# Optimization experiments

Hardware: AMD Instinct MI355X
Metric: run time of the kernel (lower is better)

Reference implementation:

```python
import jax, jax.numpy as jnp
import numpy as np

OUTPUT_SIZES = [1, 3, 6, 8]  # SPP pyramid -> total KV length 110

def _bounds(n, out):
    # PyTorch AdaptiveMaxPool2d bin boundaries
    return [((i * n) // out, -((-(i + 1) * n) // out)) for i in range(out)]

def adaptive_max_pool2d(x, out):
    # x: [B, C, H, W] -> [B, C, out, out]
    B, C, H, W = x.shape
    rows = jnp.stack([x[:, :, s:e, :].max(axis=2) for s, e in _bounds(H, out)], axis=2)
    return jnp.stack([rows[:, :, :, s:e].max(axis=3) for s, e in _bounds(W, out)], axis=3)

def spp(x):
    # [B, C, H, W] -> [B, C, S] with S = sum(o*o) = 110
    B, C = x.shape[:2]
    return jnp.concatenate(
        [adaptive_max_pool2d(x, o).reshape(B, C, o * o) for o in OUTPUT_SIZES], axis=2)

def conv1x1(x, w):
    # 1x1 conv, no bias: w [O, C], x [B, C, H, W]
    return jnp.einsum('oc,bchw->bohw', w, x)

def setup_inputs() -> dict:
    key = jax.random.key(0)
    ks = jax.random.split(key, 6)
    B, C, H, W = 16, 512, 64, 64
    IC = C // 2
    x = jax.random.normal(ks[0], (B, C, H, W), jnp.float32)
    y = jax.random.normal(ks[1], (B, C, H, W), jnp.float32)
    sc = 1.0 / np.sqrt(C)
    w_phi = jax.random.normal(ks[2], (IC, C), jnp.float32) * sc
    w_theta = jax.random.normal(ks[3], (IC, C), jnp.float32) * sc
    w_g = jax.random.normal(ks[4], (IC, C), jnp.float32) * sc
    w_mask = jax.random.normal(ks[5], (C, IC), jnp.float32) * (1.0 / np.sqrt(IC))
    return {"x": x, "y": y, "w_phi": w_phi, "w_theta": w_theta,
            "w_g": w_g, "w_mask": w_mask}

def reference(x, y, w_phi, w_theta, w_g, w_mask):
    B, C, H, W = x.shape
    IC = w_phi.shape[0]
    N = H * W
    # Query: [B, N, IC]
    x_phi = conv1x1(x, w_phi).reshape(B, IC, N).transpose(0, 2, 1)
    # Keys/values from SPP-pooled y: [B, IC, S] / [B, S, IC]
    y_theta = spp(conv1x1(y, w_theta))
    y_g = spp(conv1x1(y, w_g)).transpose(0, 2, 1)
    # Attention with softmax over the QUERY axis (dim=1), as in the source
    attn = jax.nn.softmax(jnp.einsum('bnc,bcs->bns', x_phi, y_theta), axis=1)
    agg = jnp.einsum('bns,bsc->bnc', attn, y_g)          # [B, N, IC]
    agg = agg.transpose(0, 2, 1).reshape(B, IC, H, W)     # [B, IC, H, W]
    mask = conv1x1(agg, w_mask)                           # [B, C, H, W]
    return mask + x
```

## Files before the change

### kernel.cpp

```cpp
#include <hip/hip_runtime.h>

#define DI __device__ __forceinline__

typedef __attribute__((ext_vector_type(8))) __bf16 bf16x8;
typedef __attribute__((ext_vector_type(4))) float f32x4;

DI unsigned short f2bf(float x) {
  union { float f; unsigned u; } v; v.f = x;
  unsigned r = v.u + 0x7fffu + ((v.u >> 16) & 1u);
  return (unsigned short)(r >> 16);
}
DI float bf2f(unsigned short h) {
  union { unsigned u; float f; } v; v.u = ((unsigned)h) << 16;
  return v.f;
}
DI unsigned pack2(float a, float b) {
  return (unsigned)f2bf(a) | (((unsigned)f2bf(b)) << 16);
}

DI void gl_lds16(const void* g, void* l) {
  __builtin_amdgcn_global_load_lds(
      (const __attribute__((address_space(1))) void*)g,
      (__attribute__((address_space(3))) void*)l, 16, 0, 0);
}

__global__ __launch_bounds__(256) void p0w_transpose(
    const float* __restrict__ src, unsigned short* __restrict__ dst,
    const float* __restrict__ w_theta, const float* __restrict__ w_g,
    unsigned short* __restrict__ wTG)
{
  if (blockIdx.z == 16) {
    if (blockIdx.y < 2) {
      int e = ((blockIdx.y * 64 + blockIdx.x) * 256 + threadIdx.x) * 8;
      const float* s = (e < 131072) ? (w_theta + e) : (w_g + (e - 131072));
      float4 a = *(const float4*)s;
      float4 c = *(const float4*)(s + 4);
      uint4 u;
      u.x = pack2(a.x, a.y); u.y = pack2(a.z, a.w);
      u.z = pack2(c.x, c.y); u.w = pack2(c.z, c.w);
      *(uint4*)(wTG + e) = u;
    }
    return;
  }
  const int n0 = blockIdx.x * 64, c0 = blockIdx.y * 64, b = blockIdx.z;
  const int tid = threadIdx.x;
  __shared__ float T[64 * 65];
  #pragma unroll
  for (int p = 0; p < 4; ++p) {
    int r = p * 16 + (tid >> 4);
    int n4 = (tid & 15) << 2;
    *(float4*)&T[r * 65 + n4] =
        *(const float4*)(src + ((size_t)(b * 512 + c0 + r)) * 4096 + n0 + n4);
  }
  __syncthreads();
  int n = tid >> 2, cc = (tid & 3) * 16;
  unsigned u[8];
  #pragma unroll
  for (int j = 0; j < 16; j += 2)
    u[j >> 1] = pack2(T[(cc + j) * 65 + n], T[(cc + j + 1) * 65 + n]);
  unsigned short* d = dst + ((size_t)(b * 4096 + n0 + n)) * 512 + c0 + cc;
  *(uint4*)(d) = make_uint4(u[0], u[1], u[2], u[3]);
  *(uint4*)(d + 8) = make_uint4(u[4], u[5], u[6], u[7]);
}

__constant__ int c_RS[18] = {0, 0,21,42, 0,10,21,32,42,53, 0,8,16,24,32,40,48,56};
__constant__ int c_RE[18] = {64, 22,43,64, 11,22,32,43,54,64, 8,16,24,32,40,48,56,64};

__global__ __launch_bounds__(256) void k1f_conv_pool(
    const unsigned short* __restrict__ yT, const unsigned short* __restrict__ wTG,
    unsigned short* __restrict__ Rbuf)
{
  const int tid = threadIdx.x;
  const int id = blockIdx.x;
  const int tile = (id & 7) * 16 + (id >> 3);
  const int mb = (tile & 3) * 128;
  const int nbt = tile >> 2;
  const int nb = nbt * 128;
  const int b  = blockIdx.y;
  const int lane = tid & 63, wv = tid >> 6;
  const int wm = (wv & 1) * 64, wn = (wv >> 1) * 64;
  const int l15 = lane & 15, l4 = lane >> 4;

  __shared__ __align__(16) char smem[33280];
  float* P = (float*)smem;

  f32x4 acc[4][4];
  #pragma unroll
  for (int i = 0; i < 4; ++i)
    #pragma unroll
    for (int j = 0; j < 4; ++j) acc[i][j] = f32x4{0.f, 0.f, 0.f, 0.f};

  auto stage = [&](int buf, int kb) {
    unsigned short* As = (unsigned short*)(smem + buf * 16384);
    unsigned short* Bs = As + 4096;
    #pragma unroll
    for (int p = 0; p < 2; ++p) {
      int chunk = (wv * 2 + p) * 64 + lane;
      int row = chunk >> 2, c16 = chunk & 3;
      gl_lds16(wTG + ((size_t)(mb + row)) * 512 + kb + c16 * 8,
               As + (wv * 2 + p) * 512);
      gl_lds16(yT + ((size_t)(b * 4096 + nb + row)) * 512 + kb + c16 * 8,
               Bs + (wv * 2 + p) * 512);
    }
  };

  stage(0, 0);
  __syncthreads();
  int cur = 0;
  for (int t = 0; t < 16; ++t) {
    if (t < 15) stage(cur ^ 1, (t + 1) * 32);
    const unsigned short* As = (const unsigned short*)(smem + cur * 16384);
    const unsigned short* Bs = As + 4096;
    bf16x8 af[4], bfr[4];
    #pragma unroll
    for (int i = 0; i < 4; ++i)
      af[i] = *(const bf16x8*)&As[(wm + i * 16 + l15) * 32 + l4 * 8];
    #pragma unroll
    for (int j = 0; j < 4; ++j)
      bfr[j] = *(const bf16x8*)&Bs[(wn + j * 16 + l15) * 32 + l4 * 8];
    #pragma unroll
    for (int i = 0; i < 4; ++i)
      #pragma unroll
      for (int j = 0; j < 4; ++j)
        acc[i][j] = __builtin_amdgcn_mfma_f32_16x16x32_bf16(af[i], bfr[j], acc[i][j], 0, 0, 0);
    __syncthreads();
    cur ^= 1;
  }

  const int hloc = wv >> 1;
  #pragma unroll
  for (int pass = 0; pass < 2; ++pass) {
    __syncthreads();
    if (hloc == pass) {
      #pragma unroll
      for (int i = 0; i < 4; ++i)
        #pragma unroll
        for (int j = 0; j < 4; ++j)
          #pragma unroll
          for (int r = 0; r < 4; ++r)
            P[(wm + i * 16 + l4 * 4 + r) * 65 + j * 16 + l15] = acc[i][j][r];
    }
    __syncthreads();
    const int o = tid & 127;
    size_t rbase = (((size_t)(b * 64 + nbt * 2 + pass)) * 18) * 512 + mb + o;
    if (tid < 128) {
      float b0 = -3.4e38f, b1 = b0, b2 = b0, b3 = b0;
      #pragma unroll
      for (int w = 0; w < 64; ++w) {
        float v = P[o * 65 + w];
        b0 = fmaxf(b0, v);
        if (w < 22) b1 = fmaxf(b1, v);
        if (w >= 21 && w < 43) b2 = fmaxf(b2, v);
        if (w >= 42) b3 = fmaxf(b3, v);
      }
      Rbuf[rbase]           = f2bf(b0);
      Rbuf[rbase + 512]     = f2bf(b1);
      Rbuf[rbase + 2 * 512] = f2bf(b2);
      Rbuf[rbase + 3 * 512] = f2bf(b3);
    } else {
      float s6[6], s8[8];
      #pragma unroll
      for (int i = 0; i < 6; ++i) s6[i] = -3.4e38f;
      #pragma unroll
      for (int i = 0; i < 8; ++i) s8[i] = -3.4e38f;
      constexpr int R6S[6] = {0, 10, 21, 32, 42, 53};
      constexpr int R6E[6] = {11, 22, 32, 43, 54, 64};
      #pragma unroll
      for (int w = 0; w < 64; ++w) {
        float v = P[o * 65 + w];
        #pragma unroll
        for (int i = 0; i < 6; ++i)
          if (w >= R6S[i] && w < R6E[i]) s6[i] = fmaxf(s6[i], v);
        s8[w >> 3] = fmaxf(s8[w >> 3], v);
      }
      #pragma unroll
      for (int i = 0; i < 6; ++i) Rbuf[rbase + (size_t)(4 + i) * 512] = f2bf(s6[i]);
      #pragma unroll
      for (int i = 0; i < 8; ++i) Rbuf[rbase + (size_t)(10 + i) * 512] = f2bf(s8[i]);
    }
  }
}

__global__ __launch_bounds__(256) void k2_pool_final(
    const unsigned short* __restrict__ Rbuf, float* __restrict__ Pt,
    float* __restrict__ Pg)
{
  const int s = blockIdx.x, b = blockIdx.y, tid = threadIdx.x;
  size_t obase = ((size_t)(b * 128) + s) * 256 + tid;
  if (s >= 110) { Pt[obase] = 0.f; Pg[obase] = 0.f; return; }
  int he, wb;
  if (s == 0)      { he = 0; wb = 0; }
  else if (s < 10) { int i = s - 1;  he = 1 + i / 3;  wb = 1 + i % 3; }
  else if (s < 46) { int i = s - 10; he = 4 + i / 6;  wb = 4 + i % 6; }
  else             { int i = s - 46; he = 10 + i / 8; wb = 10 + i % 8; }
  float m0 = -3.4e38f, m1 = -3.4e38f;
  int e = c_RE[he];
  for (int h = c_RS[he]; h < e; ++h) {
    const unsigned short* r = Rbuf + (((size_t)(b * 64 + h)) * 18 + wb) * 512;
    m0 = fmaxf(m0, bf2f(r[tid]));
    m1 = fmaxf(m1, bf2f(r[tid + 256]));
  }
  Pt[obase] = m0;
  Pg[obase] = m1;
}

__global__ __launch_bounds__(256) void k3_fused(
    const float* __restrict__ Pt, const float* __restrict__ Pg,
    const float* __restrict__ w_phi, const float* __restrict__ w_mask,
    unsigned short* __restrict__ Kth, unsigned short* __restrict__ Ktl,
    unsigned short* __restrict__ Vb)
{
  __shared__ __align__(16) char sm3[51200];
  const int tid = threadIdx.x;
  const int tx = tid & 15, ty = tid >> 4;
  const int b = blockIdx.y;
  if (blockIdx.z == 0) {
    const int ct = blockIdx.x;
    const int c0 = tx * 4, s0 = ty * 8;
    float* Ls = (float*)sm3;
    float* Ws = Ls + 128 * 64;
    float acc[8][4] = {};
    for (int kc = 0; kc < 256; kc += 64) {
      #pragma unroll
      for (int j = 0; j < 8; ++j) {
        int flat = tid + 256 * j;
        int row = flat >> 4, k4 = (flat & 15) << 2;
        *(float4*)&Ls[row * 64 + k4] =
            *(const float4*)(Pt + ((size_t)(b * 128) + row) * 256 + kc + k4);
      }
      #pragma unroll
      for (int j = 0; j < 4; ++j) {
        int flat = tid + 256 * j;
        int row = flat >> 4, c4 = (flat & 15) << 2;
        *(float4*)&Ws[row * 68 + c4] =
            *(const float4*)(w_phi + (size_t)(kc + row) * 512 + ct * 64 + c4);
      }
      __syncthreads();
      for (int k = 0; k < 64; k += 4) {
        float4 wv[4];
        #pragma unroll
        for (int kk = 0; kk < 4; ++kk) wv[kk] = *(const float4*)&Ws[(k + kk) * 68 + c0];
        #pragma unroll
        for (int i = 0; i < 8; ++i) {
          float4 a = *(const float4*)&Ls[(s0 + i) * 64 + k];
          const float* ap = (const float*)&a;
          #pragma unroll
          for (int kk = 0; kk < 4; ++kk) {
            const float* wp = (const float*)&wv[kk];
            acc[i][0] += ap[kk] * wp[0];
            acc[i][1] += ap[kk] * wp[1];
            acc[i][2] += ap[kk] * wp[2];
            acc[i][3] += ap[kk] * wp[3];
          }
        }
      }
      __syncthreads();
    }
    #pragma unroll
    for (int i = 0; i < 8; ++i) {
      unsigned short hi[4]; float lo[4];
      #pragma unroll
      for (int j = 0; j < 4; ++j) { hi[j] = f2bf(acc[i][j]); lo[j] = acc[i][j] - bf2f(hi[j]); }
      size_t base = ((size_t)(b * 128) + s0 + i) * 512 + ct * 64 + c0;
      uint2 uh; uh.x = (unsigned)hi[0] | ((unsigned)hi[1] << 16);
      uh.y = (unsigned)hi[2] | ((unsigned)hi[3] << 16);
      uint2 ul; ul.x = pack2(lo[0], lo[1]); ul.y = pack2(lo[2], lo[3]);
      *(uint2*)&Kth[base] = uh;
      *(uint2*)&Ktl[base] = ul;
    }
  } else {
    const int ot = blockIdx.x;
    const int o0 = ty * 4;
    float* Ws = (float*)sm3;
    float* Ps = Ws + 64 * 64;
    float acc[4][8] = {};
    for (int kc = 0; kc < 256; kc += 64) {
      #pragma unroll
      for (int j = 0; j < 4; ++j) {
        int flat = tid + 256 * j;
        int row = flat >> 4, k4 = (flat & 15) << 2;
        *(float4*)&Ws[row * 64 + k4] =
            *(const float4*)(w_mask + (size_t)(ot * 64 + row) * 256 + kc + k4);
      }
      #pragma unroll
      for (int j = 0; j < 8; ++j) {
        int flat = tid + 256 * j;
        int row = flat >> 4, k4 = (flat & 15) << 2;
        *(float4*)&Ps[row * 68 + k4] =
            *(const float4*)(Pg + ((size_t)(b * 128) + row) * 256 + kc + k4);
      }
      __syncthreads();
      for (int k = 0; k < 64; k += 4) {
        float4 wv[4];
        #pragma unroll
        for (int i = 0; i < 4; ++i) wv[i] = *(const float4*)&Ws[(o0 + i) * 64 + k];
        #pragma unroll
        for (int jj = 0; jj < 8; ++jj) {
          float4 pv = *(const float4*)&Ps[(tx + 16 * jj) * 68 + k];
          const float* pp = (const float*)&pv;
          #pragma unroll
          for (int i = 0; i < 4; ++i) {
            const float* wp = (const float*)&wv[i];
            #pragma unroll
            for (int kk = 0; kk < 4; ++kk) acc[i][jj] += wp[kk] * pp[kk];
          }
        }
      }
      __syncthreads();
    }
    #pragma unroll
    for (int i = 0; i < 4; ++i)
      #pragma unroll
      for (int jj = 0; jj < 8; ++jj)
        Vb[((size_t)(b * 512) + ot * 64 + o0 + i) * 128 + tx + 16 * jj] =
            f2bf(acc[i][jj]);
  }
}

__global__ __launch_bounds__(256) void k4_scores(
    const float* __restrict__ x, const unsigned short* __restrict__ Kth,
    const unsigned short* __restrict__ Ktl, float* __restrict__ scoresT,
    float* __restrict__ pmax_g, float* __restrict__ psum_g)
{
  const int tid = threadIdx.x;
  const int ntile = blockIdx.x;
  const int nb = ntile * 128;
  const int b = blockIdx.y;
  const int lane = tid & 63, wv = tid >> 6;
  const int wm = (wv & 1) * 64, wn = (wv >> 1) * 64;
  const int l15 = lane & 15, l4 = lane >> 4;
  __shared__ __align__(16) char smem4[2 * 26624];
  __shared__ float SmP[256], SsP[256];

  const int xn = tid & 127, xh = tid >> 7;
  const float* xcol = x + ((size_t)(b * 512 + xh * 16)) * 4096 + nb + xn;

  f32x4 acc[4][4];
  #pragma unroll
  for (int i = 0; i < 4; ++i)
    #pragma unroll
    for (int j = 0; j < 4; ++j) acc[i][j] = f32x4{0.f, 0.f, 0.f, 0.f};

  float xr[16];
  auto xload = [&](int kb) {
    const float* p = xcol + (size_t)kb * 4096;
    #pragma unroll
    for (int k = 0; k < 16; ++k) xr[k] = p[(size_t)k * 4096];
  };
  auto dmaA = [&](int buf, int kb) {
    unsigned short* Ah = (unsigned short*)(smem4 + buf * 26624);
    unsigned short* Al = Ah + 4096;
    #pragma unroll
    for (int p = 0; p < 2; ++p) {
      int chunk = (wv * 2 + p) * 64 + lane;
      int row = chunk >> 2, c16 = chunk & 3;
      size_t g = ((size_t)(b * 128) + row) * 512 + kb + c16 * 8;
      gl_lds16(Kth + g, Ah + (wv * 2 + p) * 512);
      gl_lds16(Ktl + g, Al + (wv * 2 + p) * 512);
    }
  };
  auto bwrite = [&](int buf) {
    unsigned short* Bs = (unsigned short*)(smem4 + buf * 26624 + 16384);
    unsigned u[8];
    #pragma unroll
    for (int k = 0; k < 16; k += 2) u[k >> 1] = pack2(xr[k], xr[k + 1]);
    uint4* d = (uint4*)&Bs[xn * 40 + xh * 16];
    d[0] = make_uint4(u[0], u[1], u[2], u[3]);
    d[1] = make_uint4(u[4], u[5], u[6], u[7]);
  };

  xload(0);
  dmaA(0, 0);
  bwrite(0);
  __syncthreads();
  int cur = 0;
  for (int t = 0; t < 16; ++t) {
    if (t < 15) { xload((t + 1) * 32); dmaA(cur ^ 1, (t + 1) * 32); }
    const unsigned short* Ah = (const unsigned short*)(smem4 + cur * 26624);
    const unsigned short* Al = Ah + 4096;
    const unsigned short* Bs = (const unsigned short*)(smem4 + cur * 26624 + 16384);
    bf16x8 ah[4], al[4], bfr[4];
    #pragma unroll
    for (int i = 0; i < 4; ++i) {
      ah[i] = *(const bf16x8*)&Ah[(wm + i * 16 + l15) * 32 + l4 * 8];
      al[i] = *(const bf16x8*)&Al[(wm + i * 16 + l15) * 32 + l4 * 8];
    }
    #pragma unroll
    for (int j = 0; j < 4; ++j)
      bfr[j] = *(const bf16x8*)&Bs[(wn + j * 16 + l15) * 40 + l4 * 8];
    #pragma unroll
    for (int i = 0; i < 4; ++i)
      #pragma unroll
      for (int j = 0; j < 4; ++j) {
        acc[i][j] = __builtin_amdgcn_mfma_f32_16x16x32_bf16(ah[i], bfr[j], acc[i][j], 0, 0, 0);
        acc[i][j] = __builtin_amdgcn_mfma_f32_16x16x32_bf16(al[i], bfr[j], acc[i][j], 0, 0, 0);
      }
    if (t < 15) bwrite(cur ^ 1);
    __syncthreads();
    cur ^= 1;
  }

  #pragma unroll
  for (int i = 0; i < 4; ++i)
    #pragma unroll
    for (int j = 0; j < 4; ++j)
      *(float4*)(scoresT + ((size_t)(b * 4096) + nb + wn + j * 16 + l15) * 128 +
                 wm + i * 16 + l4 * 4) = *(float4*)&acc[i][j];

  const int nh = wn >> 6;
  float cm[4][4];
  #pragma unroll
  for (int i = 0; i < 4; ++i)
    #pragma unroll
    for (int r = 0; r < 4; ++r) {
      float v = fmaxf(fmaxf(acc[i][0][r], acc[i][1][r]),
                      fmaxf(acc[i][2][r], acc[i][3][r]));
      v = fmaxf(v, __shfl_xor(v, 1));
      v = fmaxf(v, __shfl_xor(v, 2));
      v = fmaxf(v, __shfl_xor(v, 4));
      v = fmaxf(v, __shfl_xor(v, 8));
      if (l15 == 0) SmP[(wm + i * 16 + l4 * 4 + r) * 2 + nh] = v;
    }
  __syncthreads();
  #pragma unroll
  for (int i = 0; i < 4; ++i)
    #pragma unroll
    for (int r = 0; r < 4; ++r) {
      int s = wm + i * 16 + l4 * 4 + r;
      cm[i][r] = fmaxf(SmP[s * 2], SmP[s * 2 + 1]);
    }
  #pragma unroll
  for (int i = 0; i < 4; ++i)
    #pragma unroll
    for (int r = 0; r < 4; ++r) {
      float s0 = __expf(acc[i][0][r] - cm[i][r]) + __expf(acc[i][1][r] - cm[i][r]) +
                 __expf(acc[i][2][r] - cm[i][r]) + __expf(acc[i][3][r] - cm[i][r]);
      s0 += __shfl_xor(s0, 1);
      s0 += __shfl_xor(s0, 2);
      s0 += __shfl_xor(s0, 4);
      s0 += __shfl_xor(s0, 8);
      if (l15 == 0) SsP[(wm + i * 16 + l4 * 4 + r) * 2 + nh] = s0;
    }
  __syncthreads();
  if (tid < 128) {
    size_t pidx = ((size_t)(b * 128) + tid) * 32 + ntile;
    pmax_g[pidx] = fmaxf(SmP[tid * 2], SmP[tid * 2 + 1]);
    psum_g[pidx] = SsP[tid * 2] + SsP[tid * 2 + 1];
  }
}

__global__ __launch_bounds__(256) void k5e_exp(
    const float* __restrict__ scoresT, const float* __restrict__ pmax_g,
    const float* __restrict__ psum_g, unsigned short* __restrict__ Eb)
{
  const int b = blockIdx.y, tid = threadIdx.x;
  __shared__ float sm[128], sl[128];
  if (tid < 128) {
    float M = 0.f, linv = 0.f;
    if (tid < 110) {
      const float* pm = pmax_g + ((size_t)(b * 128) + tid) * 32;
      const float* ps = psum_g + ((size_t)(b * 128) + tid) * 32;
      M = -3.4e38f;
      #pragma unroll
      for (int t = 0; t < 32; ++t) M = fmaxf(M, pm[t]);
      float S = 0.f;
      #pragma unroll
      for (int t = 0; t < 32; ++t) S += ps[t] * __expf(pm[t] - M);
      linv = 1.f / S;
    }
    sm[tid] = M; sl[tid] = linv;
  }
  __syncthreads();
  const size_t base = (size_t)b * 4096 * 128;
  #pragma unroll
  for (int j = 0; j < 8; ++j) {
    int chunk = blockIdx.x * 2048 + j * 256 + tid;
    int sc = (chunk & 31) * 4;
    float4 v = *(const float4*)(scoresT + base + (size_t)chunk * 4);
    float e0 = __expf(v.x - sm[sc])     * sl[sc];
    float e1 = __expf(v.y - sm[sc + 1]) * sl[sc + 1];
    float e2 = __expf(v.z - sm[sc + 2]) * sl[sc + 2];
    float e3 = __expf(v.w - sm[sc + 3]) * sl[sc + 3];
    uint2 u; u.x = pack2(e0, e1); u.y = pack2(e2, e3);
    *(uint2*)(Eb + base + (size_t)chunk * 4) = u;
  }
}

__global__ __launch_bounds__(256) void k6_out(
    const unsigned short* __restrict__ Eb, const unsigned short* __restrict__ Vb,
    const float* __restrict__ x, float* __restrict__ out)
{
  const int tid = threadIdx.x;
  const int nb = blockIdx.x * 128;
  const int mb = blockIdx.y * 128;
  const int b = blockIdx.z;
  const int lane = tid & 63, wv = tid >> 6;
  const int wm = (wv & 1) * 64, wn = (wv >> 1) * 64;
  const int l15 = lane & 15, l4 = lane >> 4;
  __shared__ __align__(16) unsigned short SA[4][4096];
  __shared__ __align__(16) unsigned short SB[4][4096];

  #pragma unroll
  for (int h = 0; h < 4; ++h)
    #pragma unroll
    for (int p = 0; p < 2; ++p) {
      int chunk = (wv * 2 + p) * 64 + lane;
      int row = chunk >> 2, c16 = chunk & 3;
      gl_lds16(Vb + ((size_t)(b * 512) + mb + row) * 128 + h * 32 + c16 * 8,
               &SA[h][(wv * 2 + p) * 512]);
      gl_lds16(Eb + ((size_t)(b * 4096) + nb + row) * 128 + h * 32 + c16 * 8,
               &SB[h][(wv * 2 + p) * 512]);
    }

  float xr[4][4][4];
  #pragma unroll
  for (int i = 0; i < 4; ++i)
    #pragma unroll
    for (int j = 0; j < 4; ++j)
      #pragma unroll
      for (int r = 0; r < 4; ++r)
        xr[i][j][r] = x[((size_t)(b * 512) + mb + wm + i * 16 + l4 * 4 + r) * 4096 +
                        nb + wn + j * 16 + l15];

  f32x4 acc[4][4];
  #pragma unroll
  for (int i = 0; i < 4; ++i)
    #pragma unroll
    for (int j = 0; j < 4; ++j) acc[i][j] = f32x4{0.f, 0.f, 0.f, 0.f};

  __syncthreads();
  #pragma unroll
  for (int h = 0; h < 4; ++h) {
    bf16x8 af[4], bfr[4];
    #pragma unroll
    for (int i = 0; i < 4; ++i)
      af[i] = *(const bf16x8*)&SA[h][(wm + i * 16 + l15) * 32 + l4 * 8];
    #pragma unroll
    for (int j = 0; j < 4; ++j)
      bfr[j] = *(const bf16x8*)&SB[h][(wn + j * 16 + l15) * 32 + l4 * 8];
    #pragma unroll
    for (int i = 0; i < 4; ++i)
      #pragma unroll
      for (int j = 0; j < 4; ++j)
        acc[i][j] = __builtin_amdgcn_mfma_f32_16x16x32_bf16(af[i], bfr[j], acc[i][j], 0, 0, 0);
  }
  #pragma unroll
  for (int i = 0; i < 4; ++i)
    #pragma unroll
    for (int j = 0; j < 4; ++j)
      #pragma unroll
      for (int r = 0; r < 4; ++r) {
        int o = mb + wm + i * 16 + l4 * 4 + r;
        size_t idx = ((size_t)(b * 512) + o) * 4096 + nb + wn + j * 16 + l15;
        out[idx] = acc[i][j][r] + xr[i][j][r];
      }
}

extern "C" void kernel_launch(void* const* d_in, const int* in_sizes, int n_in,
                              void* d_out, int out_size, void* d_ws, size_t ws_size,
                              hipStream_t stream)
{
  (void)in_sizes; (void)n_in; (void)out_size; (void)ws_size;
  const float* x       = (const float*)d_in[0];
  const float* y       = (const float*)d_in[1];
  const float* w_phi   = (const float*)d_in[2];
  const float* w_theta = (const float*)d_in[3];
  const float* w_g     = (const float*)d_in[4];
  const float* w_mask  = (const float*)d_in[5];
  float* out = (float*)d_out;

  char* ws = (char*)d_ws;
  unsigned short* yT = (unsigned short*)ws;
  char* B0 = ws + 67108864;
  unsigned short* Rbuf = (unsigned short*)B0;
  float* scoresT = (float*)B0;
  unsigned short* Eb = (unsigned short*)(B0 + 33554432);
  unsigned short* wTG = (unsigned short*)(B0 + 50331648);
  unsigned short* Vb  = (unsigned short*)(B0 + 50331648);
  float* pmax_g = (float*)(B0 + 52428800);
  float* psum_g = (float*)(B0 + 52690944);
  char* C0 = B0 + 54525952;
  float* Pt = (float*)C0;
  float* Pg = (float*)(C0 + 2097152);
  unsigned short* Kth = (unsigned short*)(C0 + 4194304);
  unsigned short* Ktl = (unsigned short*)(C0 + 6291456);

  p0w_transpose<<<dim3(64, 8, 17), 256, 0, stream>>>(y, yT, w_theta, w_g, wTG);
  k1f_conv_pool<<<dim3(128, 16), 256, 0, stream>>>(yT, wTG, Rbuf);
  k2_pool_final<<<dim3(128, 16), 256, 0, stream>>>(Rbuf, Pt, Pg);
  k3_fused<<<dim3(8, 16, 2), 256, 0, stream>>>(Pt, Pg, w_phi, w_mask, Kth, Ktl, Vb);
  k4_scores<<<dim3(32, 16), 256, 0, stream>>>(x, Kth, Ktl, scoresT, pmax_g, psum_g);
  k5e_exp<<<dim3(64, 16), 256, 0, stream>>>(scoresT, pmax_g, psum_g, Eb);
  k6_out<<<dim3(32, 4, 16), 256, 0, stream>>>(Eb, Vb, x, out);
}
```

Baseline: 490.4 us.

## Fuse y transpose/convert into conv-pool GEMM and double-buffer register prefetch

The separate pass that transposed y to bf16 in workspace is removed. k1f now loads fp32 y columns directly into registers, packs them to bf16 and writes them into padded LDS, the same way k4 already handles x. Both k1f and k4 gain a two-deep register prefetch (xrA/xrB), so global loads for step t+2 are issued before the MFMAs of step t. k6 switches to a swizzled 1D tile ordering for L2 locality. This saves writing and re-reading a 64MB bf16 copy of y, at the cost of more registers per thread and strided fp32 global loads.

```diff
diff --git a/kernel.cpp b/kernel.cpp
--- a/kernel.cpp
+++ b/kernel.cpp
@@ -24,50 +24,25 @@
       (__attribute__((address_space(3))) void*)l, 16, 0, 0);
 }
 
-__global__ __launch_bounds__(256) void p0w_transpose(
-    const float* __restrict__ src, unsigned short* __restrict__ dst,
+__global__ __launch_bounds__(256) void pw_conv(
     const float* __restrict__ w_theta, const float* __restrict__ w_g,
     unsigned short* __restrict__ wTG)
 {
-  if (blockIdx.z == 16) {
-    if (blockIdx.y < 2) {
-      int e = ((blockIdx.y * 64 + blockIdx.x) * 256 + threadIdx.x) * 8;
-      const float* s = (e < 131072) ? (w_theta + e) : (w_g + (e - 131072));
-      float4 a = *(const float4*)s;
-      float4 c = *(const float4*)(s + 4);
-      uint4 u;
-      u.x = pack2(a.x, a.y); u.y = pack2(a.z, a.w);
-      u.z = pack2(c.x, c.y); u.w = pack2(c.z, c.w);
-      *(uint4*)(wTG + e) = u;
-    }
-    return;
-  }
-  const int n0 = blockIdx.x * 64, c0 = blockIdx.y * 64, b = blockIdx.z;
-  const int tid = threadIdx.x;
-  __shared__ float T[64 * 65];
-  #pragma unroll
-  for (int p = 0; p < 4; ++p) {
-    int r = p * 16 + (tid >> 4);
-    int n4 = (tid & 15) << 2;
-    *(float4*)&T[r * 65 + n4] =
-        *(const float4*)(src + ((size_t)(b * 512 + c0 + r)) * 4096 + n0 + n4);
-  }
-  __syncthreads();
-  int n = tid >> 2, cc = (tid & 3) * 16;
-  unsigned u[8];
-  #pragma unroll
-  for (int j = 0; j < 16; j += 2)
-    u[j >> 1] = pack2(T[(cc + j) * 65 + n], T[(cc + j + 1) * 65 + n]);
-  unsigned short* d = dst + ((size_t)(b * 4096 + n0 + n)) * 512 + c0 + cc;
-  *(uint4*)(d) = make_uint4(u[0], u[1], u[2], u[3]);
-  *(uint4*)(d + 8) = make_uint4(u[4], u[5], u[6], u[7]);
+  int e = (blockIdx.x * 256 + threadIdx.x) * 8;
+  const float* src = (e < 131072) ? (w_theta + e) : (w_g + (e - 131072));
+  float4 a = *(const float4*)src;
+  float4 c = *(const float4*)(src + 4);
+  uint4 u;
+  u.x = pack2(a.x, a.y); u.y = pack2(a.z, a.w);
+  u.z = pack2(c.x, c.y); u.w = pack2(c.z, c.w);
+  *(uint4*)(wTG + e) = u;
 }
 
 __constant__ int c_RS[18] = {0, 0,21,42, 0,10,21,32,42,53, 0,8,16,24,32,40,48,56};
 __constant__ int c_RE[18] = {64, 22,43,64, 11,22,32,43,54,64, 8,16,24,32,40,48,56,64};
 
 __global__ __launch_bounds__(256) void k1f_conv_pool(
-    const unsigned short* __restrict__ yT, const unsigned short* __restrict__ wTG,
+    const float* __restrict__ y, const unsigned short* __restrict__ wTG,
     unsigned short* __restrict__ Rbuf)
 {
   const int tid = threadIdx.x;
@@ -81,35 +56,45 @@
   const int wm = (wv & 1) * 64, wn = (wv >> 1) * 64;
   const int l15 = lane & 15, l4 = lane >> 4;
 
-  __shared__ __align__(16) char smem[33280];
+  __shared__ __align__(16) char smem[2 * 18432];
   float* P = (float*)smem;
 
+  const int xn = tid & 127, xh = tid >> 7;
+  const float* ycol = y + ((size_t)(b * 512 + xh * 16)) * 4096 + nb + xn;
+
   f32x4 acc[4][4];
   #pragma unroll
   for (int i = 0; i < 4; ++i)
     #pragma unroll
     for (int j = 0; j < 4; ++j) acc[i][j] = f32x4{0.f, 0.f, 0.f, 0.f};
 
-  auto stage = [&](int buf, int kb) {
-    unsigned short* As = (unsigned short*)(smem + buf * 16384);
-    unsigned short* Bs = As + 4096;
+  float xrA[16], xrB[16];
+  auto yload = [&](float* xr, int kb) {
+    const float* p = ycol + (size_t)kb * 4096;
+    #pragma unroll
+    for (int k = 0; k < 16; ++k) xr[k] = p[(size_t)k * 4096];
+  };
+  auto dmaA = [&](int buf, int kb) {
+    unsigned short* As = (unsigned short*)(smem + buf * 18432);
     #pragma unroll
     for (int p = 0; p < 2; ++p) {
       int chunk = (wv * 2 + p) * 64 + lane;
       int row = chunk >> 2, c16 = chunk & 3;
       gl_lds16(wTG + ((size_t)(mb + row)) * 512 + kb + c16 * 8,
                As + (wv * 2 + p) * 512);
-      gl_lds16(yT + ((size_t)(b * 4096 + nb + row)) * 512 + kb + c16 * 8,
-               Bs + (wv * 2 + p) * 512);
-    }
-  };
-
-  stage(0, 0);
-  __syncthreads();
-  int cur = 0;
-  for (int t = 0; t < 16; ++t) {
-    if (t < 15) stage(cur ^ 1, (t + 1) * 32);
-    const unsigned short* As = (const unsigned short*)(smem + cur * 16384);
+    }
+  };
+  auto bwrite = [&](int buf, const float* xr) {
+    unsigned short* Bs = (unsigned short*)(smem + buf * 18432 + 8192);
+    unsigned u[8];
+    #pragma unroll
+    for (int k = 0; k < 16; k += 2) u[k >> 1] = pack2(xr[k], xr[k + 1]);
+    uint4* d = (uint4*)&Bs[xn * 40 + xh * 16];
+    d[0] = make_uint4(u[0], u[1], u[2], u[3]);
+    d[1] = make_uint4(u[4], u[5], u[6], u[7]);
+  };
+  auto mfma_step = [&](int buf) {
+    const unsigned short* As = (const unsigned short*)(smem + buf * 18432);
     const unsigned short* Bs = As + 4096;
     bf16x8 af[4], bfr[4];
     #pragma unroll
@@ -117,14 +102,29 @@
       af[i] = *(const bf16x8*)&As[(wm + i * 16 + l15) * 32 + l4 * 8];
     #pragma unroll
     for (int j = 0; j < 4; ++j)
-      bfr[j] = *(const bf16x8*)&Bs[(wn + j * 16 + l15) * 32 + l4 * 8];
+      bfr[j] = *(const bf16x8*)&Bs[(wn + j * 16 + l15) * 40 + l4 * 8];
     #pragma unroll
     for (int i = 0; i < 4; ++i)
       #pragma unroll
       for (int j = 0; j < 4; ++j)
         acc[i][j] = __builtin_amdgcn_mfma_f32_16x16x32_bf16(af[i], bfr[j], acc[i][j], 0, 0, 0);
+  };
+
+  yload(xrA, 0);
+  dmaA(0, 0);
+  bwrite(0, xrA);
+  yload(xrB, 32);
+  __syncthreads();
+  for (int t = 0; t < 16; t += 2) {
+    dmaA(1, (t + 1) * 32);
+    bwrite(1, xrB);
+    if (t + 2 < 16) yload(xrA, (t + 2) * 32);
+    mfma_step(0);
     __syncthreads();
-    cur ^= 1;
+    if (t + 2 < 16) { dmaA(0, (t + 2) * 32); bwrite(0, xrA); }
+    if (t + 3 < 16) yload(xrB, (t + 3) * 32);
+    mfma_step(1);
+    __syncthreads();
   }
 
   const int hloc = wv >> 1;
@@ -341,8 +341,8 @@
     #pragma unroll
     for (int j = 0; j < 4; ++j) acc[i][j] = f32x4{0.f, 0.f, 0.f, 0.f};
 
-  float xr[16];
-  auto xload = [&](int kb) {
+  float xrA[16], xrB[16];
+  auto xload = [&](float* xr, int kb) {
     const float* p = xcol + (size_t)kb * 4096;
     #pragma unroll
     for (int k = 0; k < 16; ++k) xr[k] = p[(size_t)k * 4096];
@@ -359,7 +359,7 @@
       gl_lds16(Ktl + g, Al + (wv * 2 + p) * 512);
     }
   };
-  auto bwrite = [&](int buf) {
+  auto bwrite = [&](int buf, const float* xr) {
     unsigned short* Bs = (unsigned short*)(smem4 + buf * 26624 + 16384);
     unsigned u[8];
     #pragma unroll
@@ -368,17 +368,10 @@
     d[0] = make_uint4(u[0], u[1], u[2], u[3]);
     d[1] = make_uint4(u[4], u[5], u[6], u[7]);
   };
-
-  xload(0);
-  dmaA(0, 0);
-  bwrite(0);
-  __syncthreads();
-  int cur = 0;
-  for (int t = 0; t < 16; ++t) {
-    if (t < 15) { xload((t + 1) * 32); dmaA(cur ^ 1, (t + 1) * 32); }
-    const unsigned short* Ah = (const unsigned short*)(smem4 + cur * 26624);
+  auto mfma_step = [&](int buf) {
+    const unsigned short* Ah = (const unsigned short*)(smem4 + buf * 26624);
     const unsigned short* Al = Ah + 4096;
-    const unsigned short* Bs = (const unsigned short*)(smem4 + cur * 26624 + 16384);
+    const unsigned short* Bs = Al + 4096;
     bf16x8 ah[4], al[4], bfr[4];
     #pragma unroll
     for (int i = 0; i < 4; ++i) {
@@ -395,9 +388,23 @@
         acc[i][j] = __builtin_amdgcn_mfma_f32_16x16x32_bf16(ah[i], bfr[j], acc[i][j], 0, 0, 0);
         acc[i][j] = __builtin_amdgcn_mfma_f32_16x16x32_bf16(al[i], bfr[j], acc[i][j], 0, 0, 0);
       }
-    if (t < 15) bwrite(cur ^ 1);
+  };
+
+  xload(xrA, 0);
+  dmaA(0, 0);
+  bwrite(0, xrA);
+  xload(xrB, 32);
+  __syncthreads();
+  for (int t = 0; t < 16; t += 2) {
+    dmaA(1, (t + 1) * 32);
+    bwrite(1, xrB);
+    if (t + 2 < 16) xload(xrA, (t + 2) * 32);
+    mfma_step(0);
     __syncthreads();
-    cur ^= 1;
+    if (t + 2 < 16) { dmaA(0, (t + 2) * 32); bwrite(0, xrA); }
+    if (t + 3 < 16) xload(xrB, (t + 3) * 32);
+    mfma_step(1);
+    __syncthreads();
   }
 
   #pragma unroll
@@ -491,9 +498,11 @@
     const float* __restrict__ x, float* __restrict__ out)
 {
   const int tid = threadIdx.x;
-  const int nb = blockIdx.x * 128;
-  const int mb = blockIdx.y * 128;
-  const int b = blockIdx.z;
+  const int id = blockIdx.x;
+  const int tile = (id & 7) * 16 + (id >> 3);
+  const int mb = (tile & 3) * 128;
+  const int nb = (tile >> 2) * 128;
+  const int b = blockIdx.y;
   const int lane = tid & 63, wv = tid >> 6;
   const int wm = (wv & 1) * 64, wn = (wv >> 1) * 64;
   const int l15 = lane & 15, l4 = lane >> 4;
@@ -570,7 +579,6 @@
   float* out = (float*)d_out;
 
   char* ws = (char*)d_ws;
-  unsigned short* yT = (unsigned short*)ws;
   char* B0 = ws + 67108864;
   unsigned short* Rbuf = (unsigned short*)B0;
   float* scoresT = (float*)B0;
@@ -585,11 +593,11 @@
   unsigned short* Kth = (unsigned short*)(C0 + 4194304);
   unsigned short* Ktl = (unsigned short*)(C0 + 6291456);
 
-  p0w_transpose<<<dim3(64, 8, 17), 256, 0, stream>>>(y, yT, w_theta, w_g, wTG);
-  k1f_conv_pool<<<dim3(128, 16), 256, 0, stream>>>(yT, wTG, Rbuf);
+  pw_conv<<<dim3(128), 256, 0, stream>>>(w_theta, w_g, wTG);
+  k1f_conv_pool<<<dim3(128, 16), 256, 0, stream>>>(y, wTG, Rbuf);
   k2_pool_final<<<dim3(128, 16), 256, 0, stream>>>(Rbuf, Pt, Pg);
   k3_fused<<<dim3(8, 16, 2), 256, 0, stream>>>(Pt, Pg, w_phi, w_mask, Kth, Ktl, Vb);
   k4_scores<<<dim3(32, 16), 256, 0, stream>>>(x, Kth, Ktl, scoresT, pmax_g, psum_g);
   k5e_exp<<<dim3(64, 16), 256, 0, stream>>>(scoresT, pmax_g, psum_g, Eb);
-  k6_out<<<dim3(32, 4, 16), 256, 0, stream>>>(Eb, Vb, x, out);
-}
+  k6_out<<<dim3(128, 16), 256, 0, stream>>>(Eb, Vb, x, out);
+}
```

Result: no change. 487.4 us (-0.6%).
